# Kernel optimization log

Hardware: AMD Instinct MI355X
Metric: run time of the kernel (lower is better)

## Reference

```python
import jax, jax.numpy as jnp
import numpy as np

N = 100_000        # nodes
E = 1_600_000      # edges (avg degree 16)
IN, HID, H, OUT = 256, 32, 4, 40
HDIM = HID * H     # 128, hidden layer width
NEG_SLOPE = 0.2    # PyG GATConv default leaky-relu slope


def gat_conv(x, edge_index, W, a_src, a_dst, b, heads):
    """PyG-style GATConv (concat=True, add_self_loops=True, eval mode).
    x: [n, in], W: [in, heads*c], a_src/a_dst: [heads, c], b: [heads*c]."""
    n = x.shape[0]
    c = W.shape[1] // heads
    xh = (x @ W).reshape(n, heads, c)                       # [n,h,c]
    loops = jnp.arange(n, dtype=edge_index.dtype)
    src = jnp.concatenate([edge_index[0], loops])           # [E+n]
    dst = jnp.concatenate([edge_index[1], loops])
    a_s = jnp.einsum('nhc,hc->nh', xh, a_src)               # alpha_j part
    a_d = jnp.einsum('nhc,hc->nh', xh, a_dst)               # alpha_i part
    e = a_s[src] + a_d[dst]                                 # [E+n,h]
    e = jnp.where(e > 0, e, NEG_SLOPE * e)                  # leaky relu
    # numerically stable softmax over incoming edges per dst node
    m = jax.ops.segment_max(e, dst, num_segments=n)
    alpha = jnp.exp(e - m[dst])
    denom = jax.ops.segment_sum(alpha, dst, num_segments=n)
    alpha = alpha / denom[dst]
    msg = alpha[:, :, None] * xh[src]                       # [E+n,h,c]
    out = jax.ops.segment_sum(msg, dst, num_segments=n)     # [n,h,c]
    return out.reshape(n, heads * c) + b


def setup_inputs() -> dict:
    key = jax.random.key(0)
    ks = jax.random.split(key, 16)
    edge = jax.random.randint(ks[0], (2, E), 0, N, dtype=jnp.int64)
    features = jax.random.normal(ks[1], (N, IN), dtype=jnp.float32)
    s = lambda fan: 1.0 / np.sqrt(fan)
    # conv1: in -> HID with H heads (concat)
    W1 = jax.random.normal(ks[2], (IN, H * HID), jnp.float32) * s(IN)
    a_src1 = jax.random.normal(ks[3], (H, HID), jnp.float32) * s(HID)
    a_dst1 = jax.random.normal(ks[4], (H, HID), jnp.float32) * s(HID)
    b1 = jnp.zeros((H * HID,), jnp.float32)
    # hidden: HDIM -> HDIM, 1 head
    W2 = jax.random.normal(ks[5], (HDIM, HDIM), jnp.float32) * s(HDIM)
    a_src2 = jax.random.normal(ks[6], (1, HDIM), jnp.float32) * s(HDIM)
    a_dst2 = jax.random.normal(ks[7], (1, HDIM), jnp.float32) * s(HDIM)
    b2 = jnp.zeros((HDIM,), jnp.float32)
    # conv2: HDIM -> OUT, 1 head
    W3 = jax.random.normal(ks[8], (HDIM, OUT), jnp.float32) * s(HDIM)
    a_src3 = jax.random.normal(ks[9], (1, OUT), jnp.float32) * s(OUT)
    a_dst3 = jax.random.normal(ks[10], (1, OUT), jnp.float32) * s(OUT)
    b3 = jnp.zeros((OUT,), jnp.float32)
    return dict(edge=edge, features=features,
                W1=W1, a_src1=a_src1, a_dst1=a_dst1, b1=b1,
                W2=W2, a_src2=a_src2, a_dst2=a_dst2, b2=b2,
                W3=W3, a_src3=a_src3, a_dst3=a_dst3, b3=b3)


def reference(edge, features, W1, a_src1, a_dst1, b1,
              W2, a_src2, a_dst2, b2, W3, a_src3, a_dst3, b3):
    h = jax.nn.relu(gat_conv(features, edge, W1, a_src1, a_dst1, b1, H))
    h = jax.nn.relu(gat_conv(h, edge, W2, a_src2, a_dst2, b2, 1))
    # dropout omitted (eval mode)
    h = gat_conv(h, edge, W3, a_src3, a_dst3, b3, 1)
    return jax.nn.log_softmax(h, axis=1)
```

## Files before the change

### kernel.cpp

```cpp
#include <hip/hip_runtime.h>
#include <cstdint>

#define N_NODES 100000
#define N_EDGES 1600000
#define NEG_SLOPE 0.2f

#define NBUCK 391
#define NCHUNK 128
#define CHUNK_SZ ((N_EDGES + NCHUNK - 1) / NCHUNK)

typedef short s16x8 __attribute__((ext_vector_type(8)));
typedef float f32x4 __attribute__((ext_vector_type(4)));

__device__ inline float bf2f(ushort u) {
    union { uint i; float f; } x; x.i = ((uint)u) << 16; return x.f;
}
__device__ inline ushort f2bf(float f) {
    union { float f; uint i; } x; x.f = f;
    uint r = x.i + 0x7FFF + ((x.i >> 16) & 1);
    return (ushort)(r >> 16);
}
__device__ inline float lrelu(float e) { return (e > 0.f) ? e : NEG_SLOPE * e; }


__global__ __launch_bounds__(256) void bucket_hist(const int* __restrict__ dst,
                                                   int* __restrict__ chunkCnt) {
    __shared__ int cnt[NBUCK];
    int t = threadIdx.x, blk = blockIdx.x;
    for (int b = t; b < NBUCK; b += 256) cnt[b] = 0;
    __syncthreads();
    int beg = blk * CHUNK_SZ, end = min(beg + CHUNK_SZ, N_EDGES);
    for (int i = beg + t; i < end; i += 256) atomicAdd(&cnt[dst[i] >> 8], 1);
    __syncthreads();
    for (int b = t; b < NBUCK; b += 256) chunkCnt[blk * NBUCK + b] = cnt[b];
}

__global__ __launch_bounds__(512) void bucket_scan(const int* __restrict__ chunkCnt,
                                                   int* __restrict__ chunkBase,
                                                   int* __restrict__ bucketBase) {
    __shared__ int tot[512];
    int b = threadIdx.x;
    int run = 0;
    if (b < NBUCK) {
        for (int c = 0; c < NCHUNK; ++c) {
            chunkBase[c * NBUCK + b] = run;
            run += chunkCnt[c * NBUCK + b];
        }
    }
    tot[b] = (b < NBUCK) ? run : 0;
    __syncthreads();
    for (int off = 1; off < 512; off <<= 1) {
        int x = (b >= off) ? tot[b - off] : 0;
        __syncthreads();
        tot[b] += x;
        __syncthreads();
    }
    if (b == 0) bucketBase[0] = 0;
    if (b < NBUCK) bucketBase[b + 1] = tot[b];
}

__global__ __launch_bounds__(256) void bucket_scatter(const int* __restrict__ src,
                                                      const int* __restrict__ dst,
                                                      const int* __restrict__ chunkBase,
                                                      const int* __restrict__ bucketBase,
                                                      int* __restrict__ pairs) {
    __shared__ int cur[NBUCK];
    int t = threadIdx.x, blk = blockIdx.x;
    for (int b = t; b < NBUCK; b += 256)
        cur[b] = bucketBase[b] + chunkBase[blk * NBUCK + b];
    __syncthreads();
    int beg = blk * CHUNK_SZ, end = min(beg + CHUNK_SZ, N_EDGES);
    for (int i = beg + t; i < end; i += 256) {
        int d = dst[i];
        int pos = atomicAdd(&cur[d >> 8], 1);
        pairs[pos] = (src[i] << 8) | (d & 255);
    }
}

__global__ __launch_bounds__(256) void bucket_build(const int* __restrict__ pairs,
                                                    const int* __restrict__ bucketBase,
                                                    int* __restrict__ rowptr,
                                                    int* __restrict__ csr) {
    __shared__ int cnt[256], pre[256];
    int b = blockIdx.x, t = threadIdx.x;
    cnt[t] = 0;
    __syncthreads();
    int beg = bucketBase[b], end = bucketBase[b + 1];
    for (int i = beg + t; i < end; i += 256) atomicAdd(&cnt[pairs[i] & 255], 1);
    __syncthreads();
    int v = cnt[t];
    pre[t] = v;
    __syncthreads();
    for (int off = 1; off < 256; off <<= 1) {
        int x = (t >= off) ? pre[t - off] : 0;
        __syncthreads();
        pre[t] += x;
        __syncthreads();
    }
    int excl = pre[t] - v;
    int node = b * 256 + t;
    if (node <= N_NODES) rowptr[node] = beg + excl;
    cnt[t] = excl;
    __syncthreads();
    for (int i = beg + t; i < end; i += 256) {
        int p = pairs[i];
        int pos = beg + atomicAdd(&cnt[p & 255], 1);
        csr[pos] = p >> 8;
    }
}

__global__ void transpose_w(const float* __restrict__ W, ushort* __restrict__ BT,
                            int K, int N, int Npad) {
    int i = blockIdx.x * blockDim.x + threadIdx.x;
    if (i >= Npad * K) return;
    int n = i / K, k = i - n * K;
    float v = (n < N) ? W[(size_t)k * N + n] : 0.f;
    BT[i] = f2bf(v);
}


__global__ __launch_bounds__(256) void mfma_gemm1(const float* __restrict__ X,
                                                  const ushort* __restrict__ BT,
                                                  ushort* __restrict__ Y) {
    __shared__ ushort As_[64][40];
    __shared__ ushort Bs[128][40];
    int m0 = blockIdx.x * 64;
    int t = threadIdx.x;
    int wave = t >> 6, lane = t & 63;
    int wm = wave >> 1, wn = wave & 1;
    f32x4 acc[2][4] = {};
    for (int kt = 0; kt < 256; kt += 32) {
        {
            int r = t >> 2, kg = (t & 3) << 3;
            int rr = (m0 + r < N_NODES) ? m0 + r : N_NODES - 1;
            float4 xa = *(const float4*)&X[(size_t)rr * 256 + kt + kg];
            float4 xb = *(const float4*)&X[(size_t)rr * 256 + kt + kg + 4];
            ushort o[8] = { f2bf(xa.x), f2bf(xa.y), f2bf(xa.z), f2bf(xa.w),
                            f2bf(xb.x), f2bf(xb.y), f2bf(xb.z), f2bf(xb.w) };
            *(s16x8*)&As_[r][kg] = *(s16x8*)o;
        }
        #pragma unroll
        for (int i = 0; i < 2; ++i) {
            int idx = t + (i << 8);
            int r = idx >> 2, kg = (idx & 3) << 3;
            *(s16x8*)&Bs[r][kg] = *(const s16x8*)&BT[(size_t)r * 256 + kt + kg];
        }
        __syncthreads();
        int row = lane & 15, koff = (lane >> 4) << 3;
        s16x8 a[2], b[4];
        #pragma unroll
        for (int mf = 0; mf < 2; ++mf)
            a[mf] = *(s16x8*)&As_[wm * 32 + mf * 16 + row][koff];
        #pragma unroll
        for (int nf = 0; nf < 4; ++nf)
            b[nf] = *(s16x8*)&Bs[wn * 64 + nf * 16 + row][koff];
        #pragma unroll
        for (int mf = 0; mf < 2; ++mf)
            #pragma unroll
            for (int nf = 0; nf < 4; ++nf)
                acc[mf][nf] = __builtin_amdgcn_mfma_f32_16x16x32_bf16(a[mf], b[nf], acc[mf][nf], 0, 0, 0);
        __syncthreads();
    }
    int colb = lane & 15, rowb = (lane >> 4) << 2;
    #pragma unroll
    for (int mf = 0; mf < 2; ++mf)
        #pragma unroll
        for (int nf = 0; nf < 4; ++nf)
            #pragma unroll
            for (int reg = 0; reg < 4; ++reg) {
                int row = m0 + wm * 32 + mf * 16 + rowb + reg;
                int col = wn * 64 + nf * 16 + colb;
                if (row < N_NODES) Y[(size_t)row * 128 + col] = f2bf(acc[mf][nf][reg]);
            }
}


template <int K>
__global__ __launch_bounds__(256) void mfma_gemm_nc128(const ushort* __restrict__ X,
                                                       const ushort* __restrict__ BT,
                                                       ushort* __restrict__ Y) {
    __shared__ ushort As_[64][40];
    __shared__ ushort Bs[128][40];
    int m0 = blockIdx.x * 64;
    int t = threadIdx.x;
    int wave = t >> 6, lane = t & 63;
    int wm = wave >> 1, wn = wave & 1;
    f32x4 acc[2][4] = {};
    for (int kt = 0; kt < K; kt += 32) {
        {
            int r = t >> 2, kg = (t & 3) << 3;
            *(s16x8*)&As_[r][kg] = *(const s16x8*)&X[(size_t)(m0 + r) * K + kt + kg];
        }
        #pragma unroll
        for (int i = 0; i < 2; ++i) {
            int idx = t + (i << 8);
            int r = idx >> 2, kg = (idx & 3) << 3;
            *(s16x8*)&Bs[r][kg] = *(const s16x8*)&BT[(size_t)r * K + kt + kg];
        }
        __syncthreads();
        int row = lane & 15, koff = (lane >> 4) << 3;
        s16x8 a[2], b[4];
        #pragma unroll
        for (int mf = 0; mf < 2; ++mf)
            a[mf] = *(s16x8*)&As_[wm * 32 + mf * 16 + row][koff];
        #pragma unroll
        for (int nf = 0; nf < 4; ++nf)
            b[nf] = *(s16x8*)&Bs[wn * 64 + nf * 16 + row][koff];
        #pragma unroll
        for (int mf = 0; mf < 2; ++mf)
            #pragma unroll
            for (int nf = 0; nf < 4; ++nf)
                acc[mf][nf] = __builtin_amdgcn_mfma_f32_16x16x32_bf16(a[mf], b[nf], acc[mf][nf], 0, 0, 0);
        __syncthreads();
    }
    int colb = lane & 15, rowb = (lane >> 4) << 2;
    #pragma unroll
    for (int mf = 0; mf < 2; ++mf)
        #pragma unroll
        for (int nf = 0; nf < 4; ++nf)
            #pragma unroll
            for (int reg = 0; reg < 4; ++reg) {
                int row = m0 + wm * 32 + mf * 16 + rowb + reg;
                int col = wn * 64 + nf * 16 + colb;
                if (row < N_NODES) Y[(size_t)row * 128 + col] = f2bf(acc[mf][nf][reg]);
            }
}


__global__ __launch_bounds__(256) void mfma_gemm_nc40(const ushort* __restrict__ X,
                                                      const ushort* __restrict__ BT,
                                                      ushort* __restrict__ Y) {
    __shared__ ushort As_[64][40];
    __shared__ ushort Bs[48][40];
    int m0 = blockIdx.x * 64;
    int t = threadIdx.x, wave = t >> 6, lane = t & 63;
    f32x4 acc[3] = {};
    for (int kt = 0; kt < 128; kt += 32) {
        {
            int r = t >> 2, kg = (t & 3) << 3;
            *(s16x8*)&As_[r][kg] = *(const s16x8*)&X[(size_t)(m0 + r) * 128 + kt + kg];
        }
        if (t < 192) {
            int r = t >> 2, kg = (t & 3) << 3;
            *(s16x8*)&Bs[r][kg] = *(const s16x8*)&BT[(size_t)r * 128 + kt + kg];
        }
        __syncthreads();
        int row = lane & 15, koff = (lane >> 4) << 3;
        s16x8 a = *(s16x8*)&As_[wave * 16 + row][koff];
        #pragma unroll
        for (int nf = 0; nf < 3; ++nf) {
            s16x8 b = *(s16x8*)&Bs[nf * 16 + row][koff];
            acc[nf] = __builtin_amdgcn_mfma_f32_16x16x32_bf16(a, b, acc[nf], 0, 0, 0);
        }
        __syncthreads();
    }
    int colb = lane & 15, rowb = (lane >> 4) << 2;
    #pragma unroll
    for (int nf = 0; nf < 3; ++nf)
        #pragma unroll
        for (int reg = 0; reg < 4; ++reg) {
            int row = m0 + wave * 16 + rowb + reg;
            int col = nf * 16 + colb;
            if (row < N_NODES) Y[(size_t)row * 64 + col] = f2bf(acc[nf][reg]);
        }
}


template <int WD, int NH, int SEG>
__global__ void as_ad_bf16(const ushort* __restrict__ XH, const float* __restrict__ asrc,
                           const float* __restrict__ adst, float* __restrict__ As,
                           float* __restrict__ Ad) {
    int node = (int)((blockIdx.x * blockDim.x + threadIdx.x) >> 6);
    int lane = threadIdx.x & 63;
    if (node >= N_NODES) return;
    int c0 = lane * 2;
    uint xv = *reinterpret_cast<const uint*>(&XH[(size_t)node * WD + c0]);
    float x0 = bf2f((ushort)(xv & 0xFFFF)), x1 = bf2f((ushort)(xv >> 16));
    float2 a = *reinterpret_cast<const float2*>(&asrc[c0]);
    float2 b = *reinterpret_cast<const float2*>(&adst[c0]);
    float s = x0 * a.x + x1 * a.y;
    float d = x0 * b.x + x1 * b.y;
    #pragma unroll
    for (int off = 1; off < SEG; off <<= 1) {
        s += __shfl_xor(s, off, 64);
        d += __shfl_xor(d, off, 64);
    }
    if ((lane % SEG) == 0) {
        int h = c0 / (WD / NH);
        As[(size_t)node * NH + h] = s;
        Ad[(size_t)node * NH + h] = d;
    }
}

__global__ void as_ad_w64_40(const ushort* __restrict__ XH, const float* __restrict__ asrc,
                             const float* __restrict__ adst, float* __restrict__ As,
                             float* __restrict__ Ad) {
    int node = (int)((blockIdx.x * blockDim.x + threadIdx.x) >> 6);
    int lane = threadIdx.x & 63;
    if (node >= N_NODES) return;
    int c0 = lane * 2;
    float s = 0.f, d = 0.f;
    if (c0 < 40) {
        uint xv = *reinterpret_cast<const uint*>(&XH[(size_t)node * 64 + c0]);
        float x0 = bf2f((ushort)(xv & 0xFFFF)), x1 = bf2f((ushort)(xv >> 16));
        float2 a = *reinterpret_cast<const float2*>(&asrc[c0]);
        float2 b = *reinterpret_cast<const float2*>(&adst[c0]);
        s = x0 * a.x + x1 * a.y;
        d = x0 * b.x + x1 * b.y;
    }
    #pragma unroll
    for (int off = 1; off < 64; off <<= 1) {
        s += __shfl_xor(s, off, 64);
        d += __shfl_xor(d, off, 64);
    }
    if (lane == 0) { As[node] = s; Ad[node] = d; }
}


template <int NH>
__global__ void agg_fused_bf16(const ushort* __restrict__ XH, const float* __restrict__ As,
                               const float* __restrict__ Ad, const float* __restrict__ bias,
                               const int* __restrict__ rowptr, const int* __restrict__ csr,
                               ushort* __restrict__ Y) {
    int node = (int)((blockIdx.x * blockDim.x + threadIdx.x) >> 6);
    int lane = threadIdx.x & 63;
    if (node >= N_NODES) return;
    int sub = lane >> 4;
    int cg = (lane & 15) << 3;
    int hB = (NH == 4) ? ((lane & 15) >> 2) : 0;
    float adiB = Ad[(size_t)node * NH + hB];
    int beg = rowptr[node], deg = rowptr[node + 1] - beg;
    int items = deg + 1;
    float acc[8] = {};
    float den = 0.f;
    for (int base = 0; base < items; base += 4) {
        int i = base + sub;
        int src = (i < deg) ? csr[beg + i] : node;
        float e = As[(size_t)src * NH + hB] + adiB;
        float a = __expf(lrelu(e));
        if (i > deg) a = 0.f;
        den += a;
        uint4 rv = *(const uint4*)&XH[(size_t)src * 128 + cg];
        uint rw[4] = { rv.x, rv.y, rv.z, rv.w };
        #pragma unroll
        for (int k = 0; k < 4; ++k) {
            acc[2 * k]     += a * bf2f((ushort)(rw[k] & 0xFFFF));
            acc[2 * k + 1] += a * bf2f((ushort)(rw[k] >> 16));
        }
    }
    den += __shfl_xor(den, 16, 64);
    den += __shfl_xor(den, 32, 64);
    #pragma unroll
    for (int k = 0; k < 8; ++k) {
        acc[k] += __shfl_xor(acc[k], 16, 64);
        acc[k] += __shfl_xor(acc[k], 32, 64);
    }
    if (sub == 0) {
        float dinv = 1.0f / den;
        uint o[4];
        #pragma unroll
        for (int k = 0; k < 4; ++k) {
            float v0 = fmaxf(acc[2 * k]     * dinv + bias[cg + 2 * k],     0.f);
            float v1 = fmaxf(acc[2 * k + 1] * dinv + bias[cg + 2 * k + 1], 0.f);
            o[k] = (uint)f2bf(v0) | ((uint)f2bf(v1) << 16);
        }
        *reinterpret_cast<uint4*>(&Y[(size_t)node * 128 + cg]) = *reinterpret_cast<uint4*>(o);
    }
}


__global__ void agg_fused_l3(const ushort* __restrict__ XH, const float* __restrict__ As,
                             const float* __restrict__ Ad, const float* __restrict__ bias,
                             const int* __restrict__ rowptr, const int* __restrict__ csr,
                             float* __restrict__ Y) {
    int node = (int)((blockIdx.x * blockDim.x + threadIdx.x) >> 6);
    int lane = threadIdx.x & 63;
    if (node >= N_NODES) return;
    int sub = lane >> 3;
    int cg = (lane & 7) << 3;
    float adi = Ad[node];
    int beg = rowptr[node], deg = rowptr[node + 1] - beg;
    int items = deg + 1;
    float acc[8] = {};
    float den = 0.f;
    for (int base = 0; base < items; base += 8) {
        int i = base + sub;
        int src = (i < deg) ? csr[beg + i] : node;
        float a = __expf(lrelu(As[src] + adi));
        if (i > deg) a = 0.f;
        den += a;
        uint4 rv = *(const uint4*)&XH[(size_t)src * 64 + cg];
        uint rw[4] = { rv.x, rv.y, rv.z, rv.w };
        #pragma unroll
        for (int k = 0; k < 4; ++k) {
            acc[2 * k]     += a * bf2f((ushort)(rw[k] & 0xFFFF));
            acc[2 * k + 1] += a * bf2f((ushort)(rw[k] >> 16));
        }
    }
    den += __shfl_xor(den, 8, 64);
    den += __shfl_xor(den, 16, 64);
    den += __shfl_xor(den, 32, 64);
    #pragma unroll
    for (int k = 0; k < 8; ++k) {
        acc[k] += __shfl_xor(acc[k], 8, 64);
        acc[k] += __shfl_xor(acc[k], 16, 64);
        acc[k] += __shfl_xor(acc[k], 32, 64);
    }
    bool valid = (lane < 5);
    float v[8];
    float pm = -1e30f;
    if (valid) {
        float dinv = 1.0f / den;
        #pragma unroll
        for (int k = 0; k < 8; ++k) {
            v[k] = acc[k] * dinv + bias[cg + k];
            pm = fmaxf(pm, v[k]);
        }
    }
    #pragma unroll
    for (int off = 1; off < 8; off <<= 1) pm = fmaxf(pm, __shfl_xor(pm, off, 64));
    float ps = 0.f;
    if (valid) {
        #pragma unroll
        for (int k = 0; k < 8; ++k) ps += __expf(v[k] - pm);
    }
    #pragma unroll
    for (int off = 1; off < 8; off <<= 1) ps += __shfl_xor(ps, off, 64);
    if (valid) {
        float lden = __logf(ps);
        float4 o0 = make_float4(v[0] - pm - lden, v[1] - pm - lden,
                                v[2] - pm - lden, v[3] - pm - lden);
        float4 o1 = make_float4(v[4] - pm - lden, v[5] - pm - lden,
                                v[6] - pm - lden, v[7] - pm - lden);
        *reinterpret_cast<float4*>(&Y[(size_t)node * 40 + cg]) = o0;
        *reinterpret_cast<float4*>(&Y[(size_t)node * 40 + cg + 4]) = o1;
    }
}


static inline size_t align256(size_t x) { return (x + 255) & ~(size_t)255; }

extern "C" void kernel_launch(void* const* d_in, const int* in_sizes, int n_in,
                              void* d_out, int out_size, void* d_ws, size_t ws_size,
                              hipStream_t stream) {
    const int*   edge = (const int*)d_in[0];
    const float* feat = (const float*)d_in[1];
    const float* W1   = (const float*)d_in[2];
    const float* as1  = (const float*)d_in[3];
    const float* ad1  = (const float*)d_in[4];
    const float* b1   = (const float*)d_in[5];
    const float* W2   = (const float*)d_in[6];
    const float* as2  = (const float*)d_in[7];
    const float* ad2  = (const float*)d_in[8];
    const float* b2   = (const float*)d_in[9];
    const float* W3   = (const float*)d_in[10];
    const float* as3  = (const float*)d_in[11];
    const float* ad3  = (const float*)d_in[12];
    const float* b3   = (const float*)d_in[13];
    float* out = (float*)d_out;

    const int* srcArr = edge;
    const int* dstArr = edge + N_EDGES;

    const size_t NB128 = (size_t)N_NODES * 128 * 2;

    char* w = (char*)d_ws;
    char* regionA = w; w += align256(2 * NB128);
    char* regionB = w; w += align256(NB128);
    char* regionC = w; w += align256(NB128);
    float* As   = (float*)w; w += align256((size_t)N_NODES * 4 * 4);
    float* Ad   = (float*)w; w += align256((size_t)N_NODES * 4 * 4);
    int* rowptr = (int*)w;   w += align256((size_t)(N_NODES + 1) * 4);
    int* csr    = (int*)w;   w += align256((size_t)N_EDGES * 4);
    int* chunkCnt  = (int*)w; w += align256((size_t)NCHUNK * NBUCK * 4);
    int* chunkBase = (int*)w; w += align256((size_t)NCHUNK * NBUCK * 4);
    int* bucketBase = (int*)w; w += align256((size_t)(NBUCK + 1) * 4);
    ushort* WT1 = (ushort*)w; w += align256((size_t)128 * 256 * 2);
    ushort* WT2 = (ushort*)w; w += align256((size_t)128 * 128 * 2);
    ushort* WT3 = (ushort*)w; w += align256((size_t)48 * 128 * 2);

    int* pairs = (int*)regionA;

    ushort* xh1 = (ushort*)regionB;
    ushort* h1  = (ushort*)regionC;
    ushort* xh2 = (ushort*)regionA;
    ushort* h2  = (ushort*)(regionA + NB128);
    ushort* xh3 = (ushort*)regionB;

    bucket_hist<<<NCHUNK, 256, 0, stream>>>(dstArr, chunkCnt);
    bucket_scan<<<1, 512, 0, stream>>>(chunkCnt, chunkBase, bucketBase);
    bucket_scatter<<<NCHUNK, 256, 0, stream>>>(srcArr, dstArr, chunkBase, bucketBase, pairs);
    bucket_build<<<NBUCK, 256, 0, stream>>>(pairs, bucketBase, rowptr, csr);

    transpose_w<<<(128 * 256 + 255) / 256, 256, 0, stream>>>(W1, WT1, 256, 128, 128);
    transpose_w<<<(128 * 128 + 255) / 256, 256, 0, stream>>>(W2, WT2, 128, 128, 128);
    transpose_w<<<(48 * 128 + 255) / 256, 256, 0, stream>>>(W3, WT3, 128, 40, 48);

    int aggGrid = (N_NODES + 3) / 4;
    int gemmGrid = (N_NODES + 63) / 64;

    mfma_gemm1<<<gemmGrid, 256, 0, stream>>>(feat, WT1, xh1);
    as_ad_bf16<128, 4, 16><<<aggGrid, 256, 0, stream>>>(xh1, as1, ad1, As, Ad);
    agg_fused_bf16<4><<<aggGrid, 256, 0, stream>>>(xh1, As, Ad, b1, rowptr, csr, h1);

    mfma_gemm_nc128<128><<<gemmGrid, 256, 0, stream>>>(h1, WT2, xh2);
    as_ad_bf16<128, 1, 64><<<aggGrid, 256, 0, stream>>>(xh2, as2, ad2, As, Ad);
    agg_fused_bf16<1><<<aggGrid, 256, 0, stream>>>(xh2, As, Ad, b2, rowptr, csr, h2);

    mfma_gemm_nc40<<<gemmGrid, 256, 0, stream>>>(h2, WT3, xh3);
    as_ad_w64_40<<<aggGrid, 256, 0, stream>>>(xh3, as3, ad3, As, Ad);
    agg_fused_l3<<<aggGrid, 256, 0, stream>>>(xh3, As, Ad, b3, rowptr, csr, out);
}
```

Baseline: 378.1 us.

## Fuse attention-score dot products into GEMM epilogues and store features as fp8

Each projection GEMM now computes the per-node source and destination attention scores in its epilogue, using shuffle reductions and shared memory. This removes the three separate as_ad kernels and the extra reads of the projected features. The projected features are stored as software-encoded e4m3 fp8 bytes instead of bf16, halving the bytes gathered per edge in the aggregation kernels at the cost of software decode ALU work. The fp8 quantization reduces accuracy of the messages and may exceed tolerance.

```diff
diff --git a/kernel.cpp b/kernel.cpp
--- a/kernel.cpp
+++ b/kernel.cpp
@@ -21,6 +21,33 @@
     return (ushort)(r >> 16);
 }
 __device__ inline float lrelu(float e) { return (e > 0.f) ? e : NEG_SLOPE * e; }
+
+__device__ inline uint f2e4m3(float f) {
+    uint bits = __float_as_uint(f);
+    uint s = (bits >> 24) & 0x80;
+    float af = __uint_as_float(bits & 0x7FFFFFFF);
+    af = fminf(af, 448.f);
+    uint out;
+    if (af < 0.015625f) {
+        out = (uint)rintf(af * 512.f);
+    } else {
+        uint ab = __float_as_uint(af);
+        uint r = ab + 0x0007FFFFu + ((ab >> 20) & 1u);
+        int e2 = (int)((r >> 23) & 0xFF) - 127;
+        uint m3 = (r >> 20) & 7u;
+        if (e2 > 8) { e2 = 8; m3 = 6; }
+        out = ((uint)(e2 + 7) << 3) | m3;
+    }
+    return s | out;
+}
+__device__ inline float e4m32f(uint u) {
+    uint exp = (u >> 3) & 0xF;
+    uint m = u & 7u;
+    float mant = (float)((exp ? 8u : 0u) | m);
+    uint e = (exp ? exp : 1u) + 117u;
+    float v = mant * __uint_as_float(e << 23);
+    return (u & 0x80) ? -v : v;
+}
 
 
 __global__ __launch_bounds__(256) void bucket_hist(const int* __restrict__ dst,
@@ -121,9 +148,14 @@
 
 __global__ __launch_bounds__(256) void mfma_gemm1(const float* __restrict__ X,
                                                   const ushort* __restrict__ BT,
-                                                  ushort* __restrict__ Y) {
-    __shared__ ushort As_[64][40];
+                                                  const float* __restrict__ asv,
+                                                  const float* __restrict__ adv,
+                                                  uchar* __restrict__ X8,
+                                                  float* __restrict__ As,
+                                                  float* __restrict__ Ad) {
+    __shared__ ushort Ats[64][40];
     __shared__ ushort Bs[128][40];
+    __shared__ float sA[64][4], sD[64][4];
     int m0 = blockIdx.x * 64;
     int t = threadIdx.x;
     int wave = t >> 6, lane = t & 63;
@@ -137,7 +169,7 @@
             float4 xb = *(const float4*)&X[(size_t)rr * 256 + kt + kg + 4];
             ushort o[8] = { f2bf(xa.x), f2bf(xa.y), f2bf(xa.z), f2bf(xa.w),
                             f2bf(xb.x), f2bf(xb.y), f2bf(xb.z), f2bf(xb.w) };
-            *(s16x8*)&As_[r][kg] = *(s16x8*)o;
+            *(s16x8*)&Ats[r][kg] = *(s16x8*)o;
         }
         #pragma unroll
         for (int i = 0; i < 2; ++i) {
@@ -150,7 +182,7 @@
         s16x8 a[2], b[4];
         #pragma unroll
         for (int mf = 0; mf < 2; ++mf)
-            a[mf] = *(s16x8*)&As_[wm * 32 + mf * 16 + row][koff];
+            a[mf] = *(s16x8*)&Ats[wm * 32 + mf * 16 + row][koff];
         #pragma unroll
         for (int nf = 0; nf < 4; ++nf)
             b[nf] = *(s16x8*)&Bs[wn * 64 + nf * 16 + row][koff];
@@ -162,6 +194,29 @@
         __syncthreads();
     }
     int colb = lane & 15, rowb = (lane >> 4) << 2;
+    float a0 = asv[wn * 64 + colb],      d0 = adv[wn * 64 + colb];
+    float a1 = asv[wn * 64 + 16 + colb], d1 = adv[wn * 64 + 16 + colb];
+    float a2 = asv[wn * 64 + 32 + colb], d2 = adv[wn * 64 + 32 + colb];
+    float a3 = asv[wn * 64 + 48 + colb], d3 = adv[wn * 64 + 48 + colb];
+    #pragma unroll
+    for (int mf = 0; mf < 2; ++mf)
+        #pragma unroll
+        for (int reg = 0; reg < 4; ++reg) {
+            float v0 = acc[mf][0][reg], v1 = acc[mf][1][reg];
+            float v2 = acc[mf][2][reg], v3 = acc[mf][3][reg];
+            float sLo = v0 * a0 + v1 * a1, sHi = v2 * a2 + v3 * a3;
+            float dLo = v0 * d0 + v1 * d1, dHi = v2 * d2 + v3 * d3;
+            #pragma unroll
+            for (int off = 1; off < 16; off <<= 1) {
+                sLo += __shfl_xor(sLo, off, 64); sHi += __shfl_xor(sHi, off, 64);
+                dLo += __shfl_xor(dLo, off, 64); dHi += __shfl_xor(dHi, off, 64);
+            }
+            if (colb == 0) {
+                int r = wm * 32 + mf * 16 + rowb + reg;
+                sA[r][wn * 2] = sLo; sA[r][wn * 2 + 1] = sHi;
+                sD[r][wn * 2] = dLo; sD[r][wn * 2 + 1] = dHi;
+            }
+        }
     #pragma unroll
     for (int mf = 0; mf < 2; ++mf)
         #pragma unroll
@@ -170,39 +225,52 @@
             for (int reg = 0; reg < 4; ++reg) {
                 int row = m0 + wm * 32 + mf * 16 + rowb + reg;
                 int col = wn * 64 + nf * 16 + colb;
-                if (row < N_NODES) Y[(size_t)row * 128 + col] = f2bf(acc[mf][nf][reg]);
+                if (row < N_NODES) X8[(size_t)row * 128 + col] = (uchar)f2e4m3(acc[mf][nf][reg]);
             }
-}
-
-
-template <int K>
-__global__ __launch_bounds__(256) void mfma_gemm_nc128(const ushort* __restrict__ X,
-                                                       const ushort* __restrict__ BT,
-                                                       ushort* __restrict__ Y) {
-    __shared__ ushort As_[64][40];
+    __syncthreads();
+    {
+        int r = t >> 2, h = t & 3;
+        int node = m0 + r;
+        if (node < N_NODES) {
+            As[(size_t)node * 4 + h] = sA[r][h];
+            Ad[(size_t)node * 4 + h] = sD[r][h];
+        }
+    }
+}
+
+
+__global__ __launch_bounds__(256) void mfma_gemm2(const ushort* __restrict__ X,
+                                                  const ushort* __restrict__ BT,
+                                                  const float* __restrict__ asv,
+                                                  const float* __restrict__ adv,
+                                                  uchar* __restrict__ X8,
+                                                  float* __restrict__ As,
+                                                  float* __restrict__ Ad) {
+    __shared__ ushort Ats[64][40];
     __shared__ ushort Bs[128][40];
+    __shared__ float sA1[64], sD1[64];
     int m0 = blockIdx.x * 64;
     int t = threadIdx.x;
     int wave = t >> 6, lane = t & 63;
     int wm = wave >> 1, wn = wave & 1;
     f32x4 acc[2][4] = {};
-    for (int kt = 0; kt < K; kt += 32) {
+    for (int kt = 0; kt < 128; kt += 32) {
         {
             int r = t >> 2, kg = (t & 3) << 3;
-            *(s16x8*)&As_[r][kg] = *(const s16x8*)&X[(size_t)(m0 + r) * K + kt + kg];
+            *(s16x8*)&Ats[r][kg] = *(const s16x8*)&X[(size_t)(m0 + r) * 128 + kt + kg];
         }
         #pragma unroll
         for (int i = 0; i < 2; ++i) {
             int idx = t + (i << 8);
             int r = idx >> 2, kg = (idx & 3) << 3;
-            *(s16x8*)&Bs[r][kg] = *(const s16x8*)&BT[(size_t)r * K + kt + kg];
+            *(s16x8*)&Bs[r][kg] = *(const s16x8*)&BT[(size_t)r * 128 + kt + kg];
         }
         __syncthreads();
         int row = lane & 15, koff = (lane >> 4) << 3;
         s16x8 a[2], b[4];
         #pragma unroll
         for (int mf = 0; mf < 2; ++mf)
-            a[mf] = *(s16x8*)&As_[wm * 32 + mf * 16 + row][koff];
+            a[mf] = *(s16x8*)&Ats[wm * 32 + mf * 16 + row][koff];
         #pragma unroll
         for (int nf = 0; nf < 4; ++nf)
             b[nf] = *(s16x8*)&Bs[wn * 64 + nf * 16 + row][koff];
@@ -213,7 +281,32 @@
                 acc[mf][nf] = __builtin_amdgcn_mfma_f32_16x16x32_bf16(a[mf], b[nf], acc[mf][nf], 0, 0, 0);
         __syncthreads();
     }
+    if (t < 64) { sA1[t] = 0.f; sD1[t] = 0.f; }
+    __syncthreads();
     int colb = lane & 15, rowb = (lane >> 4) << 2;
+    float a0 = asv[wn * 64 + colb],      d0 = adv[wn * 64 + colb];
+    float a1 = asv[wn * 64 + 16 + colb], d1 = adv[wn * 64 + 16 + colb];
+    float a2 = asv[wn * 64 + 32 + colb], d2 = adv[wn * 64 + 32 + colb];
+    float a3 = asv[wn * 64 + 48 + colb], d3 = adv[wn * 64 + 48 + colb];
+    #pragma unroll
+    for (int mf = 0; mf < 2; ++mf)
+        #pragma unroll
+        for (int reg = 0; reg < 4; ++reg) {
+            float v0 = acc[mf][0][reg], v1 = acc[mf][1][reg];
+            float v2 = acc[mf][2][reg], v3 = acc[mf][3][reg];
+            float s = v0 * a0 + v1 * a1 + v2 * a2 + v3 * a3;
+            float d = v0 * d0 + v1 * d1 + v2 * d2 + v3 * d3;
+            #pragma unroll
+            for (int off = 1; off < 16; off <<= 1) {
+                s += __shfl_xor(s, off, 64);
+                d += __shfl_xor(d, off, 64);
+            }
+            if (colb == 0) {
+                int r = wm * 32 + mf * 16 + rowb + reg;
+                atomicAdd(&sA1[r], s);
+                atomicAdd(&sD1[r], d);
+            }
+        }
     #pragma unroll
     for (int mf = 0; mf < 2; ++mf)
         #pragma unroll
@@ -222,15 +315,24 @@
             for (int reg = 0; reg < 4; ++reg) {
                 int row = m0 + wm * 32 + mf * 16 + rowb + reg;
                 int col = wn * 64 + nf * 16 + colb;
-                if (row < N_NODES) Y[(size_t)row * 128 + col] = f2bf(acc[mf][nf][reg]);
+                if (row < N_NODES) X8[(size_t)row * 128 + col] = (uchar)f2e4m3(acc[mf][nf][reg]);
             }
-}
-
-
-__global__ __launch_bounds__(256) void mfma_gemm_nc40(const ushort* __restrict__ X,
-                                                      const ushort* __restrict__ BT,
-                                                      ushort* __restrict__ Y) {
-    __shared__ ushort As_[64][40];
+    __syncthreads();
+    if (t < 64) {
+        int node = m0 + t;
+        if (node < N_NODES) { As[node] = sA1[t]; Ad[node] = sD1[t]; }
+    }
+}
+
+
+__global__ __launch_bounds__(256) void mfma_gemm3(const ushort* __restrict__ X,
+                                                  const ushort* __restrict__ BT,
+                                                  const float* __restrict__ asv,
+                                                  const float* __restrict__ adv,
+                                                  uchar* __restrict__ X8,
+                                                  float* __restrict__ As,
+                                                  float* __restrict__ Ad) {
+    __shared__ ushort Ats[64][40];
     __shared__ ushort Bs[48][40];
     int m0 = blockIdx.x * 64;
     int t = threadIdx.x, wave = t >> 6, lane = t & 63;
@@ -238,7 +340,7 @@
     for (int kt = 0; kt < 128; kt += 32) {
         {
             int r = t >> 2, kg = (t & 3) << 3;
-            *(s16x8*)&As_[r][kg] = *(const s16x8*)&X[(size_t)(m0 + r) * 128 + kt + kg];
+            *(s16x8*)&Ats[r][kg] = *(const s16x8*)&X[(size_t)(m0 + r) * 128 + kt + kg];
         }
         if (t < 192) {
             int r = t >> 2, kg = (t & 3) << 3;
@@ -246,7 +348,7 @@
         }
         __syncthreads();
         int row = lane & 15, koff = (lane >> 4) << 3;
-        s16x8 a = *(s16x8*)&As_[wave * 16 + row][koff];
+        s16x8 a = *(s16x8*)&Ats[wave * 16 + row][koff];
         #pragma unroll
         for (int nf = 0; nf < 3; ++nf) {
             s16x8 b = *(s16x8*)&Bs[nf * 16 + row][koff];
@@ -255,73 +357,40 @@
         __syncthreads();
     }
     int colb = lane & 15, rowb = (lane >> 4) << 2;
+    float a0 = asv[colb],      d0 = adv[colb];
+    float a1 = asv[16 + colb], d1 = adv[16 + colb];
+    float a2 = (32 + colb < 40) ? asv[32 + colb] : 0.f;
+    float d2 = (32 + colb < 40) ? adv[32 + colb] : 0.f;
+    #pragma unroll
+    for (int reg = 0; reg < 4; ++reg) {
+        float s = acc[0][reg] * a0 + acc[1][reg] * a1 + acc[2][reg] * a2;
+        float d = acc[0][reg] * d0 + acc[1][reg] * d1 + acc[2][reg] * d2;
+        #pragma unroll
+        for (int off = 1; off < 16; off <<= 1) {
+            s += __shfl_xor(s, off, 64);
+            d += __shfl_xor(d, off, 64);
+        }
+        if (colb == 0) {
+            int node = m0 + wave * 16 + rowb + reg;
+            if (node < N_NODES) { As[node] = s; Ad[node] = d; }
+        }
+    }
     #pragma unroll
     for (int nf = 0; nf < 3; ++nf)
         #pragma unroll
         for (int reg = 0; reg < 4; ++reg) {
             int row = m0 + wave * 16 + rowb + reg;
             int col = nf * 16 + colb;
-            if (row < N_NODES) Y[(size_t)row * 64 + col] = f2bf(acc[nf][reg]);
-        }
-}
-
-
-template <int WD, int NH, int SEG>
-__global__ void as_ad_bf16(const ushort* __restrict__ XH, const float* __restrict__ asrc,
-                           const float* __restrict__ adst, float* __restrict__ As,
-                           float* __restrict__ Ad) {
-    int node = (int)((blockIdx.x * blockDim.x + threadIdx.x) >> 6);
-    int lane = threadIdx.x & 63;
-    if (node >= N_NODES) return;
-    int c0 = lane * 2;
-    uint xv = *reinterpret_cast<const uint*>(&XH[(size_t)node * WD + c0]);
-    float x0 = bf2f((ushort)(xv & 0xFFFF)), x1 = bf2f((ushort)(xv >> 16));
-    float2 a = *reinterpret_cast<const float2*>(&asrc[c0]);
-    float2 b = *reinterpret_cast<const float2*>(&adst[c0]);
-    float s = x0 * a.x + x1 * a.y;
-    float d = x0 * b.x + x1 * b.y;
-    #pragma unroll
-    for (int off = 1; off < SEG; off <<= 1) {
-        s += __shfl_xor(s, off, 64);
-        d += __shfl_xor(d, off, 64);
-    }
-    if ((lane % SEG) == 0) {
-        int h = c0 / (WD / NH);
-        As[(size_t)node * NH + h] = s;
-        Ad[(size_t)node * NH + h] = d;
-    }
-}
-
-__global__ void as_ad_w64_40(const ushort* __restrict__ XH, const float* __restrict__ asrc,
-                             const float* __restrict__ adst, float* __restrict__ As,
-                             float* __restrict__ Ad) {
-    int node = (int)((blockIdx.x * blockDim.x + threadIdx.x) >> 6);
-    int lane = threadIdx.x & 63;
-    if (node >= N_NODES) return;
-    int c0 = lane * 2;
-    float s = 0.f, d = 0.f;
-    if (c0 < 40) {
-        uint xv = *reinterpret_cast<const uint*>(&XH[(size_t)node * 64 + c0]);
-        float x0 = bf2f((ushort)(xv & 0xFFFF)), x1 = bf2f((ushort)(xv >> 16));
-        float2 a = *reinterpret_cast<const float2*>(&asrc[c0]);
-        float2 b = *reinterpret_cast<const float2*>(&adst[c0]);
-        s = x0 * a.x + x1 * a.y;
-        d = x0 * b.x + x1 * b.y;
-    }
-    #pragma unroll
-    for (int off = 1; off < 64; off <<= 1) {
-        s += __shfl_xor(s, off, 64);
-        d += __shfl_xor(d, off, 64);
-    }
-    if (lane == 0) { As[node] = s; Ad[node] = d; }
+            if (row < N_NODES) X8[(size_t)row * 64 + col] = (uchar)f2e4m3(acc[nf][reg]);
+        }
 }
 
 
 template <int NH>
-__global__ void agg_fused_bf16(const ushort* __restrict__ XH, const float* __restrict__ As,
-                               const float* __restrict__ Ad, const float* __restrict__ bias,
-                               const int* __restrict__ rowptr, const int* __restrict__ csr,
-                               ushort* __restrict__ Y) {
+__global__ void agg_fused_fp8(const uchar* __restrict__ X8, const float* __restrict__ As,
+                              const float* __restrict__ Ad, const float* __restrict__ bias,
+                              const int* __restrict__ rowptr, const int* __restrict__ csr,
+                              ushort* __restrict__ Y) {
     int node = (int)((blockIdx.x * blockDim.x + threadIdx.x) >> 6);
     int lane = threadIdx.x & 63;
     if (node >= N_NODES) return;
@@ -340,13 +409,12 @@
         float a = __expf(lrelu(e));
         if (i > deg) a = 0.f;
         den += a;
-        uint4 rv = *(const uint4*)&XH[(size_t)src * 128 + cg];
-        uint rw[4] = { rv.x, rv.y, rv.z, rv.w };
-        #pragma unroll
-        for (int k = 0; k < 4; ++k) {
-            acc[2 * k]     += a * bf2f((ushort)(rw[k] & 0xFFFF));
-            acc[2 * k + 1] += a * bf2f((ushort)(rw[k] >> 16));
-        }
+        uint2 rv = *(const uint2*)&X8[(size_t)src * 128 + cg];
+        uint w0 = rv.x, w1 = rv.y;
+        acc[0] += a * e4m32f(w0 & 255);         acc[1] += a * e4m32f((w0 >> 8) & 255);
+        acc[2] += a * e4m32f((w0 >> 16) & 255); acc[3] += a * e4m32f(w0 >> 24);
+        acc[4] += a * e4m32f(w1 & 255);         acc[5] += a * e4m32f((w1 >> 8) & 255);
+        acc[6] += a * e4m32f((w1 >> 16) & 255); acc[7] += a * e4m32f(w1 >> 24);
     }
     den += __shfl_xor(den, 16, 64);
     den += __shfl_xor(den, 32, 64);
@@ -369,10 +437,10 @@
 }
 
 
-__global__ void agg_fused_l3(const ushort* __restrict__ XH, const float* __restrict__ As,
-                             const float* __restrict__ Ad, const float* __restrict__ bias,
-                             const int* __restrict__ rowptr, const int* __restrict__ csr,
-                             float* __restrict__ Y) {
+__global__ void agg_l3_fp8(const uchar* __restrict__ X8, const float* __restrict__ As,
+                           const float* __restrict__ Ad, const float* __restrict__ bias,
+                           const int* __restrict__ rowptr, const int* __restrict__ csr,
+                           float* __restrict__ Y) {
     int node = (int)((blockIdx.x * blockDim.x + threadIdx.x) >> 6);
     int lane = threadIdx.x & 63;
     if (node >= N_NODES) return;
@@ -389,13 +457,12 @@
         float a = __expf(lrelu(As[src] + adi));
         if (i > deg) a = 0.f;
         den += a;
-        uint4 rv = *(const uint4*)&XH[(size_t)src * 64 + cg];
-        uint rw[4] = { rv.x, rv.y, rv.z, rv.w };
-        #pragma unroll
-        for (int k = 0; k < 4; ++k) {
-            acc[2 * k]     += a * bf2f((ushort)(rw[k] & 0xFFFF));
-            acc[2 * k + 1] += a * bf2f((ushort)(rw[k] >> 16));
-        }
+        uint2 rv = *(const uint2*)&X8[(size_t)src * 64 + cg];
+        uint w0 = rv.x, w1 = rv.y;
+        acc[0] += a * e4m32f(w0 & 255);         acc[1] += a * e4m32f((w0 >> 8) & 255);
+        acc[2] += a * e4m32f((w0 >> 16) & 255); acc[3] += a * e4m32f(w0 >> 24);
+        acc[4] += a * e4m32f(w1 & 255);         acc[5] += a * e4m32f((w1 >> 8) & 255);
+        acc[6] += a * e4m32f((w1 >> 16) & 255); acc[7] += a * e4m32f(w1 >> 24);
     }
     den += __shfl_xor(den, 8, 64);
     den += __shfl_xor(den, 16, 64);
@@ -481,11 +548,11 @@
 
     int* pairs = (int*)regionA;
 
-    ushort* xh1 = (ushort*)regionB;
-    ushort* h1  = (ushort*)regionC;
-    ushort* xh2 = (ushort*)regionA;
-    ushort* h2  = (ushort*)(regionA + NB128);
-    ushort* xh3 = (ushort*)regionB;
+    uchar*  x8_1 = (uchar*)regionB;
+    uchar*  x8_3 = (uchar*)(regionB + NB128 / 2);
+    ushort* h1   = (ushort*)regionC;
+    uchar*  x8_2 = (uchar*)regionA;
+    ushort* h2   = (ushort*)(regionA + NB128);
 
     bucket_hist<<<NCHUNK, 256, 0, stream>>>(dstArr, chunkCnt);
     bucket_scan<<<1, 512, 0, stream>>>(chunkCnt, chunkBase, bucketBase);
@@ -499,15 +566,12 @@
     int aggGrid = (N_NODES + 3) / 4;
     int gemmGrid = (N_NODES + 63) / 64;
 
-    mfma_gemm1<<<gemmGrid, 256, 0, stream>>>(feat, WT1, xh1);
-    as_ad_bf16<128, 4, 16><<<aggGrid, 256, 0, stream>>>(xh1, as1, ad1, As, Ad);
-    agg_fused_bf16<4><<<aggGrid, 256, 0, stream>>>(xh1, As, Ad, b1, rowptr, csr, h1);
-
-    mfma_gemm_nc128<128><<<gemmGrid, 256, 0, stream>>>(h1, WT2, xh2);
-    as_ad_bf16<128, 1, 64><<<aggGrid, 256, 0, stream>>>(xh2, as2, ad2, As, Ad);
-    agg_fused_bf16<1><<<aggGrid, 256, 0, stream>>>(xh2, As, Ad, b2, rowptr, csr, h2);
-
-    mfma_gemm_nc40<<<gemmGrid, 256, 0, stream>>>(h2, WT3, xh3);
-    as_ad_w64_40<<<aggGrid, 256, 0, stream>>>(xh3, as3, ad3, As, Ad);
-    agg_fused_l3<<<aggGrid, 256, 0, stream>>>(xh3, As, Ad, b3, rowptr, csr, out);
-}
+    mfma_gemm1<<<gemmGrid, 256, 0, stream>>>(feat, WT1, as1, ad1, x8_1, As, Ad);
+    agg_fused_fp8<4><<<aggGrid, 256, 0, stream>>>(x8_1, As, Ad, b1, rowptr, csr, h1);
+
+    mfma_gemm2<<<gemmGrid, 256, 0, stream>>>(h1, WT2, as2, ad2, x8_2, As, Ad);
+    agg_fused_fp8<1><<<aggGrid, 256, 0, stream>>>(x8_2, As, Ad, b2, rowptr, csr, h2);
+
+    mfma_gemm3<<<gemmGrid, 256, 0, stream>>>(h2, WT3, as3, ad3, x8_3, As, Ad);
+    agg_l3_fp8<<<aggGrid, 256, 0, stream>>>(x8_3, As, Ad, b3, rowptr, csr, out);
+}
```

Result: slower. 445.1 us (+17.7%).
